# Kernel optimization log

Hardware: AMD Instinct MI355X
Metric: run time of the kernel (lower is better)

## Reference

```python
import jax, jax.numpy as jnp
import numpy as np

D_MODEL = 1024
N_HEAD = 16


def setup_inputs() -> dict:
    key = jax.random.key(0)
    ks = jax.random.split(key, 9)
    d = D_MODEL
    s = 0.02
    return {
        "x": jax.random.normal(ks[0], (4, 2048, d), dtype=jnp.float32),
        "w_q": jax.random.normal(ks[1], (d, d), dtype=jnp.float32) * s,
        "b_q": jax.random.normal(ks[2], (d,), dtype=jnp.float32) * s,
        "w_k": jax.random.normal(ks[3], (d, d), dtype=jnp.float32) * s,
        "b_k": jax.random.normal(ks[4], (d,), dtype=jnp.float32) * s,
        "w_v": jax.random.normal(ks[5], (d, d), dtype=jnp.float32) * s,
        "b_v": jax.random.normal(ks[6], (d,), dtype=jnp.float32) * s,
        "w_o": jax.random.normal(ks[7], (d, d), dtype=jnp.float32) * s,
        "b_o": jax.random.normal(ks[8], (d,), dtype=jnp.float32) * s,
    }


def reference(x, w_q, b_q, w_k, b_k, w_v, b_v, w_o, b_o):
    B, S, D = x.shape
    H = N_HEAD
    dh = D // H

    def split(t):  # [B,S,D] -> [B,H,S,dh]
        return t.reshape(B, S, H, dh).transpose(0, 2, 1, 3)

    q = split(x @ w_q + b_q)
    k = split(x @ w_k + b_k)
    v = split(x @ w_v + b_v)

    scale = 1.0 / jnp.sqrt(jnp.float32(dh))
    score = jnp.einsum("bhqd,bhkd->bhqk", q, k) * scale
    score = jax.nn.softmax(score, axis=-1)
    out = jnp.einsum("bhqk,bhkd->bhqd", score, v)
    out = out.transpose(0, 2, 1, 3).reshape(B, S, D)
    return out @ w_o + b_o
```

## Files before the change

### kernel.cpp

```cpp
#include <hip/hip_runtime.h>


typedef __bf16 bf16x8 __attribute__((ext_vector_type(8)));
typedef __bf16 bf16x4 __attribute__((ext_vector_type(4)));
typedef float f32x4 __attribute__((ext_vector_type(4)));
typedef unsigned short u16x8 __attribute__((ext_vector_type(8)));

#define SEQ 2048
#define DM 1024
#define NHEAD 16
#define MTOT 8192

__device__ __forceinline__ unsigned short f2bf(float f) {
  unsigned u = __builtin_bit_cast(unsigned, f);
  u += 0x7fffu + ((u >> 16) & 1u);
  return (unsigned short)(u >> 16);
}

__device__ __forceinline__ void async16(const void* g, void* l) {
  __builtin_amdgcn_global_load_lds(
      (const __attribute__((address_space(1))) void*)g,
      (__attribute__((address_space(3))) void*)l, 16, 0, 0);
}

__global__ __launch_bounds__(256) void k_cvt(const float* __restrict__ x,
                                             unsigned short* __restrict__ xb) {
  size_t i = ((size_t)blockIdx.x * 256 + threadIdx.x) * 8;
  float4 a = *(const float4*)(x + i);
  float4 b = *(const float4*)(x + i + 4);
  u16x8 o;
  o[0] = f2bf(a.x); o[1] = f2bf(a.y); o[2] = f2bf(a.z); o[3] = f2bf(a.w);
  o[4] = f2bf(b.x); o[5] = f2bf(b.y); o[6] = f2bf(b.z); o[7] = f2bf(b.w);
  *(u16x8*)(xb + i) = o;
}

__global__ __launch_bounds__(256) void k_wt(const float* __restrict__ w0, const float* __restrict__ w1,
                                            const float* __restrict__ w2, const float* __restrict__ w3,
                                            unsigned short* __restrict__ t0, unsigned short* __restrict__ t1,
                                            unsigned short* __restrict__ t2, unsigned short* __restrict__ t3) {
  __shared__ float t[64][65];
  int z = blockIdx.z;
  const float* w = z == 0 ? w0 : z == 1 ? w1 : z == 2 ? w2 : w3;
  unsigned short* wt = z == 0 ? t0 : z == 1 ? t1 : z == 2 ? t2 : t3;
  int nt = blockIdx.x, kt = blockIdx.y;
  int tx = threadIdx.x & 63, ty = threadIdx.x >> 6;
  for (int i = 0; i < 16; ++i) {
    int r = i * 4 + ty;
    t[r][tx] = w[(size_t)(kt * 64 + r) * DM + nt * 64 + tx];
  }
  __syncthreads();
  for (int i = 0; i < 16; ++i) {
    int r = i * 4 + ty;
    wt[(size_t)(nt * 64 + r) * DM + kt * 64 + tx] = f2bf(t[tx][r]);
  }
}

__device__ __forceinline__ void gemm_body(const unsigned short* __restrict__ A,
                                          const unsigned short* __restrict__ Bt,
                                          const float* __restrict__ bias,
                                          unsigned short* __restrict__ Cb,
                                          float* __restrict__ Cf, int bm, int bn) {
  __shared__ __align__(16) unsigned short As[128 * 64];
  __shared__ __align__(16) unsigned short Bs[128 * 64];
  const int K = DM, N = DM;
  int tid = threadIdx.x, w = tid >> 6, l = tid & 63;
  int g = l >> 4, l15 = l & 15;
  int wm = (w >> 1) * 64, wn = (w & 1) * 64;
  f32x4 acc[4][4];
#pragma unroll
  for (int mi = 0; mi < 4; ++mi)
#pragma unroll
    for (int ni = 0; ni < 4; ++ni)
#pragma unroll
      for (int e = 0; e < 4; ++e) acc[mi][ni][e] = 0.f;

  int lr8 = l >> 3, lp = l & 7;
  for (int kt = 0; kt < K / 64; ++kt) {
    __syncthreads();
#pragma unroll
    for (int i = 0; i < 4; ++i) {
      int cs = i * 4 + w;
      int row = cs * 8 + lr8;
      int c = lp ^ lr8;
      async16(A + (size_t)(bm + row) * K + kt * 64 + c * 8, &As[cs * 512]);
      async16(Bt + (size_t)(bn + row) * K + kt * 64 + c * 8, &Bs[cs * 512]);
    }
    __syncthreads();
    bf16x8 af[4][2];
#pragma unroll
    for (int mi = 0; mi < 4; ++mi)
#pragma unroll
      for (int kk = 0; kk < 2; ++kk) {
        int row = wm + mi * 16 + l15;
        af[mi][kk] = *(const bf16x8*)&As[row * 64 + (((kk * 4 + g) ^ (row & 7)) * 8)];
      }
    __builtin_amdgcn_s_setprio(1);
#pragma unroll
    for (int ni = 0; ni < 4; ++ni) {
      int row = wn + ni * 16 + l15;
      bf16x8 b0 = *(const bf16x8*)&Bs[row * 64 + (((0 + g) ^ (row & 7)) * 8)];
      bf16x8 b1 = *(const bf16x8*)&Bs[row * 64 + (((4 + g) ^ (row & 7)) * 8)];
#pragma unroll
      for (int mi = 0; mi < 4; ++mi) {
        acc[mi][ni] = __builtin_amdgcn_mfma_f32_16x16x32_bf16(af[mi][0], b0, acc[mi][ni], 0, 0, 0);
        acc[mi][ni] = __builtin_amdgcn_mfma_f32_16x16x32_bf16(af[mi][1], b1, acc[mi][ni], 0, 0, 0);
      }
    }
    __builtin_amdgcn_s_setprio(0);
  }
  float bv[4];
#pragma unroll
  for (int ni = 0; ni < 4; ++ni) bv[ni] = bias[bn + wn + ni * 16 + l15];
#pragma unroll
  for (int mi = 0; mi < 4; ++mi)
#pragma unroll
    for (int ni = 0; ni < 4; ++ni) {
      int col = bn + wn + ni * 16 + l15;
#pragma unroll
      for (int r = 0; r < 4; ++r) {
        int rowg = bm + wm + mi * 16 + g * 4 + r;
        float v = acc[mi][ni][r] + bv[ni];
        if (Cf) Cf[(size_t)rowg * N + col] = v;
        else    Cb[(size_t)rowg * N + col] = f2bf(v);
      }
    }
}

__global__ __launch_bounds__(256) void k_gemm(const unsigned short* __restrict__ A,
                                              const unsigned short* __restrict__ Bt,
                                              const float* __restrict__ bias,
                                              unsigned short* __restrict__ Cb,
                                              float* __restrict__ Cf) {
  gemm_body(A, Bt, bias, Cb, Cf, blockIdx.y * 128, blockIdx.x * 128);
}

__global__ __launch_bounds__(256) void k_gemm_qkv(const unsigned short* __restrict__ A,
                                                  const unsigned short* bt0, const unsigned short* bt1,
                                                  const unsigned short* bt2,
                                                  const float* b0, const float* b1, const float* b2,
                                                  unsigned short* o0, unsigned short* o1,
                                                  unsigned short* o2) {
  int which = blockIdx.x >> 3;
  const unsigned short* Bt = which == 0 ? bt0 : which == 1 ? bt1 : bt2;
  const float* bias = which == 0 ? b0 : which == 1 ? b1 : b2;
  unsigned short* Cb = which == 0 ? o0 : which == 1 ? o1 : o2;
  gemm_body(A, Bt, bias, Cb, nullptr, blockIdx.y * 128, (blockIdx.x & 7) * 128);
}

__global__ __launch_bounds__(256) void k_vt(const unsigned short* __restrict__ V,
                                            unsigned short* __restrict__ Vt) {
  __shared__ __align__(16) unsigned short t[64 * 64];
  int st = blockIdx.x, bh = blockIdx.y;
  int b = bh >> 4, h = bh & 15;
  int tid = threadIdx.x, w = tid >> 6, l = tid & 63;
  for (int i = 0; i < 2; ++i) {
    int cs = i * 4 + w;
    int row = cs * 8 + (l >> 3);
    int c = l & 7;
    async16(V + ((size_t)(b * SEQ + st * 64 + row) * DM + h * 64 + c * 8), &t[cs * 512]);
  }
  __syncthreads();
  for (int p = 0; p < 2; ++p) {
    int d = p * 32 + (tid >> 3);
    int cs = tid & 7;
    u16x8 o;
    for (int j = 0; j < 8; ++j) o[j] = t[(cs * 8 + j) * 64 + d];
    *(u16x8*)(Vt + ((size_t)bh * 64 + d) * SEQ + st * 64 + cs * 8) = o;
  }
}

__global__ __launch_bounds__(256) void k_attn(const unsigned short* __restrict__ Q,
                                              const unsigned short* __restrict__ Kg,
                                              const unsigned short* __restrict__ Vt,
                                              unsigned short* __restrict__ Og) {
  __shared__ __align__(16) unsigned short Ks[2][64 * 64];
  __shared__ __align__(16) unsigned short Vs[2][64 * 64];
  __shared__ __align__(16) unsigned short Ps[128 * 64];
  const float C = 0.18033688011112042f;
  const float THR = 44.3614195558365f;
  int qt = blockIdx.x, bh = blockIdx.y;
  int b = bh >> 4, h = bh & 15;
  int tid = threadIdx.x, w = tid >> 6, l = tid & 63;
  int g = l >> 4, l15 = l & 15, l7 = l15 & 7;
  int q0 = qt * 128 + w * 32;
  int lr8 = l >> 3, lp = l & 7;

  bf16x8 bq[2][2];
#pragma unroll
  for (int qi = 0; qi < 2; ++qi)
#pragma unroll
    for (int kk = 0; kk < 2; ++kk)
      bq[qi][kk] = *(const bf16x8*)(Q + ((size_t)(b * SEQ + q0 + qi * 16 + l15) * DM) +
                                    h * 64 + kk * 32 + g * 8);

  float mrow[2], lrow[2];
  f32x4 oacc[2][4];
#pragma unroll
  for (int qi = 0; qi < 2; ++qi) {
    mrow[qi] = -__builtin_inff();
    lrow[qi] = 0.f;
#pragma unroll
    for (int no = 0; no < 4; ++no)
#pragma unroll
      for (int e = 0; e < 4; ++e) oacc[qi][no][e] = 0.f;
  }

  auto stage = [&](int kt, int bufi) {
#pragma unroll
    for (int i = 0; i < 2; ++i) {
      int cs = i * 4 + w;
      int row = cs * 8 + lr8;
      int c = lp ^ lr8;
      async16(Kg + ((size_t)(b * SEQ + kt * 64 + row) * DM + h * 64 + c * 8), &Ks[bufi][cs * 512]);
      async16(Vt + ((size_t)(bh * 64 + row) * SEQ + kt * 64 + c * 8), &Vs[bufi][cs * 512]);
    }
  };

  stage(0, 0);
  __syncthreads();

  const int NT = SEQ / 64;
  for (int kt = 0; kt < NT; ++kt) {
    int cur = kt & 1;
    if (kt + 1 < NT) stage(kt + 1, cur ^ 1);

    f32x4 sacc[4][2];
#pragma unroll
    for (int ki = 0; ki < 4; ++ki)
#pragma unroll
      for (int qi = 0; qi < 2; ++qi)
#pragma unroll
        for (int e = 0; e < 4; ++e) sacc[ki][qi][e] = 0.f;
    __builtin_amdgcn_s_setprio(1);
#pragma unroll
    for (int ki = 0; ki < 4; ++ki) {
      int row = ki * 16 + l15;
      bf16x8 a0 = *(const bf16x8*)&Ks[cur][row * 64 + (((0 + g) ^ l7) * 8)];
      bf16x8 a1 = *(const bf16x8*)&Ks[cur][row * 64 + (((4 + g) ^ l7) * 8)];
#pragma unroll
      for (int qi = 0; qi < 2; ++qi) {
        sacc[ki][qi] = __builtin_amdgcn_mfma_f32_16x16x32_bf16(a0, bq[qi][0], sacc[ki][qi], 0, 0, 0);
        sacc[ki][qi] = __builtin_amdgcn_mfma_f32_16x16x32_bf16(a1, bq[qi][1], sacc[ki][qi], 0, 0, 0);
      }
    }
    __builtin_amdgcn_s_setprio(0);

    float mx[2];
#pragma unroll
    for (int qi = 0; qi < 2; ++qi) {
      float m0 = sacc[0][qi][0];
#pragma unroll
      for (int ki = 0; ki < 4; ++ki)
#pragma unroll
        for (int r = 0; r < 4; ++r) m0 = fmaxf(m0, sacc[ki][qi][r]);
      m0 = fmaxf(m0, __shfl_xor(m0, 16));
      m0 = fmaxf(m0, __shfl_xor(m0, 32));
      mx[qi] = m0;
    }
    bool need = (mx[0] > mrow[0] + THR) || (mx[1] > mrow[1] + THR);
    if (__any(need ? 1 : 0)) {
      float co[2];
#pragma unroll
      for (int qi = 0; qi < 2; ++qi) {
        float mn = fmaxf(mrow[qi], mx[qi]);
        co[qi] = __builtin_amdgcn_exp2f((mrow[qi] - mn) * C);
        mrow[qi] = mn;
        lrow[qi] *= co[qi];
      }
#pragma unroll
      for (int qi = 0; qi < 2; ++qi)
#pragma unroll
        for (int r = 0; r < 4; ++r) {
          float bc = __shfl(co[qi], g * 4 + r);
#pragma unroll
          for (int no = 0; no < 4; ++no) oacc[qi][no][r] *= bc;
        }
    }
#pragma unroll
    for (int qi = 0; qi < 2; ++qi) {
      float rs = 0.f;
      int rowg = w * 32 + qi * 16 + l15;
#pragma unroll
      for (int ki = 0; ki < 4; ++ki) {
        float p0 = __builtin_amdgcn_exp2f((sacc[ki][qi][0] - mrow[qi]) * C);
        float p1 = __builtin_amdgcn_exp2f((sacc[ki][qi][1] - mrow[qi]) * C);
        float p2 = __builtin_amdgcn_exp2f((sacc[ki][qi][2] - mrow[qi]) * C);
        float p3 = __builtin_amdgcn_exp2f((sacc[ki][qi][3] - mrow[qi]) * C);
        rs += (p0 + p1) + (p2 + p3);
        bf16x4 pk;
        pk[0] = (__bf16)p0; pk[1] = (__bf16)p1; pk[2] = (__bf16)p2; pk[3] = (__bf16)p3;
        int chunk = ki * 2 + (g >> 1);
        *(bf16x4*)&Ps[rowg * 64 + (((chunk ^ l7) << 3) + ((g & 1) << 2))] = pk;
      }
      rs += __shfl_xor(rs, 16);
      rs += __shfl_xor(rs, 32);
      lrow[qi] += rs;
    }

#pragma unroll
    for (int kk = 0; kk < 2; ++kk) {
      bf16x8 pa[2];
#pragma unroll
      for (int qi = 0; qi < 2; ++qi) {
        int rowg = w * 32 + qi * 16 + l15;
        pa[qi] = *(const bf16x8*)&Ps[rowg * 64 + (((kk * 4 + g) ^ l7) << 3)];
      }
      __builtin_amdgcn_s_setprio(1);
#pragma unroll
      for (int no = 0; no < 4; ++no) {
        int row = no * 16 + l15;
        bf16x8 bv = *(const bf16x8*)&Vs[cur][row * 64 + (((kk * 4 + g) ^ l7) * 8)];
#pragma unroll
        for (int qi = 0; qi < 2; ++qi)
          oacc[qi][no] = __builtin_amdgcn_mfma_f32_16x16x32_bf16(pa[qi], bv, oacc[qi][no], 0, 0, 0);
      }
      __builtin_amdgcn_s_setprio(0);
    }
    __syncthreads();
  }

#pragma unroll
  for (int qi = 0; qi < 2; ++qi)
#pragma unroll
    for (int r = 0; r < 4; ++r) {
      float ls = __shfl(lrow[qi], g * 4 + r);
      float inv = 1.f / ls;
      int srow = q0 + qi * 16 + g * 4 + r;
#pragma unroll
      for (int no = 0; no < 4; ++no)
        Og[(size_t)(b * SEQ + srow) * DM + h * 64 + no * 16 + l15] =
            f2bf(oacc[qi][no][r] * inv);
    }
}

extern "C" void kernel_launch(void* const* d_in, const int* in_sizes, int n_in,
                              void* d_out, int out_size, void* d_ws, size_t ws_size,
                              hipStream_t stream) {
  const float* x  = (const float*)d_in[0];
  const float* wq = (const float*)d_in[1];
  const float* bq = (const float*)d_in[2];
  const float* wk = (const float*)d_in[3];
  const float* bk = (const float*)d_in[4];
  const float* wv = (const float*)d_in[5];
  const float* bv = (const float*)d_in[6];
  const float* wo = (const float*)d_in[7];
  const float* bo = (const float*)d_in[8];

  const size_t SZ_X = (size_t)MTOT * DM * 2;
  const size_t SZ_W = (size_t)DM * DM * 2;
  char* ws = (char*)d_ws;
  size_t off = 0;
  unsigned short* xb  = (unsigned short*)(ws + off); off += SZ_X;
  unsigned short* wqT = (unsigned short*)(ws + off); off += SZ_W;
  unsigned short* wkT = (unsigned short*)(ws + off); off += SZ_W;
  unsigned short* wvT = (unsigned short*)(ws + off); off += SZ_W;
  unsigned short* woT = (unsigned short*)(ws + off); off += SZ_W;
  unsigned short* Qb  = (unsigned short*)(ws + off); off += SZ_X;
  unsigned short* Kb  = (unsigned short*)(ws + off); off += SZ_X;
  unsigned short* Vb  = (unsigned short*)(ws + off); off += SZ_X;
  unsigned short* Vtb = (unsigned short*)(ws + off); off += SZ_X;
  unsigned short* Ab  = (unsigned short*)(ws + off); off += SZ_X;
  if (ws_size < off) return;

  k_cvt<<<dim3(4096), dim3(256), 0, stream>>>(x, xb);
  k_wt<<<dim3(16, 16, 4), dim3(256), 0, stream>>>(wq, wk, wv, wo, wqT, wkT, wvT, woT);
  k_gemm_qkv<<<dim3(24, 64), dim3(256), 0, stream>>>(xb, wqT, wkT, wvT, bq, bk, bv, Qb, Kb, Vb);
  k_vt<<<dim3(32, 64), dim3(256), 0, stream>>>(Vb, Vtb);
  k_attn<<<dim3(16, 64), dim3(256), 0, stream>>>(Qb, Kb, Vtb, Ab);
  k_gemm<<<dim3(8, 64), dim3(256), 0, stream>>>(Ab, woT, bo, nullptr, (float*)d_out);
}
```

Measured before the change: 224.0 us.

## Switch attention to 32x32x16 MFMA with register-resident P via lane shuffles

Rewrites the flash-attention kernel to use 32x32x16 bf16 MFMA tiles. With that tile shape each lane owns a single query row, so the row max and row sum need fewer cross-lane shuffles. The P matrix is no longer round-tripped through shared memory; it is packed to bf16 and rearranged into the B-operand layout with xor-32 shuffles. The key loop is unrolled by two to avoid buffer index arithmetic, and the output is staged through LDS so it can be written with coalesced 16-byte stores. This trades LDS traffic and shuffle overhead for more register pressure and cross-lane shuffles.

```diff
diff --git a/kernel.cpp b/kernel.cpp
--- a/kernel.cpp
+++ b/kernel.cpp
@@ -2,9 +2,10 @@
 
 
 typedef __bf16 bf16x8 __attribute__((ext_vector_type(8)));
-typedef __bf16 bf16x4 __attribute__((ext_vector_type(4)));
 typedef float f32x4 __attribute__((ext_vector_type(4)));
+typedef float f32x16 __attribute__((ext_vector_type(16)));
 typedef unsigned short u16x8 __attribute__((ext_vector_type(8)));
+typedef unsigned u32x4 __attribute__((ext_vector_type(4)));
 
 #define SEQ 2048
 #define DM 1024
@@ -15,6 +16,12 @@
   unsigned u = __builtin_bit_cast(unsigned, f);
   u += 0x7fffu + ((u >> 16) & 1u);
   return (unsigned short)(u >> 16);
+}
+
+__device__ __forceinline__ unsigned pkbf(float lo, float hi) {
+  __bf16 a = (__bf16)lo, b = (__bf16)hi;
+  return ((unsigned)__builtin_bit_cast(unsigned short, b) << 16) |
+         __builtin_bit_cast(unsigned short, a);
 }
 
 __device__ __forceinline__ void async16(const void* g, void* l) {
@@ -173,164 +180,170 @@
                                               const unsigned short* __restrict__ Kg,
                                               const unsigned short* __restrict__ Vt,
                                               unsigned short* __restrict__ Og) {
-  __shared__ __align__(16) unsigned short Ks[2][64 * 64];
-  __shared__ __align__(16) unsigned short Vs[2][64 * 64];
-  __shared__ __align__(16) unsigned short Ps[128 * 64];
+  __shared__ __align__(16) unsigned short smem[16384];
   const float C = 0.18033688011112042f;
   const float THR = 44.3614195558365f;
   int qt = blockIdx.x, bh = blockIdx.y;
   int b = bh >> 4, h = bh & 15;
   int tid = threadIdx.x, w = tid >> 6, l = tid & 63;
-  int g = l >> 4, l15 = l & 15, l7 = l15 & 7;
-  int q0 = qt * 128 + w * 32;
+  int l31 = l & 31, hi = l >> 5, l7 = l & 7;
   int lr8 = l >> 3, lp = l & 7;
-
-  bf16x8 bq[2][2];
-#pragma unroll
-  for (int qi = 0; qi < 2; ++qi)
-#pragma unroll
-    for (int kk = 0; kk < 2; ++kk)
-      bq[qi][kk] = *(const bf16x8*)(Q + ((size_t)(b * SEQ + q0 + qi * 16 + l15) * DM) +
-                                    h * 64 + kk * 32 + g * 8);
-
-  float mrow[2], lrow[2];
-  f32x4 oacc[2][4];
-#pragma unroll
-  for (int qi = 0; qi < 2; ++qi) {
-    mrow[qi] = -__builtin_inff();
-    lrow[qi] = 0.f;
-#pragma unroll
-    for (int no = 0; no < 4; ++no)
-#pragma unroll
-      for (int e = 0; e < 4; ++e) oacc[qi][no][e] = 0.f;
-  }
-
-  auto stage = [&](int kt, int bufi) {
+  int q0w = qt * 128 + w * 32;
+  unsigned short* const ks0 = smem;
+  unsigned short* const ks1 = smem + 4096;
+  unsigned short* const vs0 = smem + 8192;
+  unsigned short* const vs1 = smem + 12288;
+
+  bf16x8 qf[4];
+#pragma unroll
+  for (int c = 0; c < 4; ++c)
+    qf[c] = *(const bf16x8*)(Q + (size_t)(b * SEQ + q0w + l31) * DM + h * 64 + c * 16 + hi * 8);
+
+  float mrow = -__builtin_inff(), lrow = 0.f;
+  f32x16 oacc[2];
+#pragma unroll
+  for (int d = 0; d < 2; ++d)
+#pragma unroll
+    for (int r = 0; r < 16; ++r) oacc[d][r] = 0.f;
+
+  auto stage = [&](int kt, unsigned short* kdst, unsigned short* vdst) {
 #pragma unroll
     for (int i = 0; i < 2; ++i) {
       int cs = i * 4 + w;
       int row = cs * 8 + lr8;
       int c = lp ^ lr8;
-      async16(Kg + ((size_t)(b * SEQ + kt * 64 + row) * DM + h * 64 + c * 8), &Ks[bufi][cs * 512]);
-      async16(Vt + ((size_t)(bh * 64 + row) * SEQ + kt * 64 + c * 8), &Vs[bufi][cs * 512]);
+      async16(Kg + ((size_t)(b * SEQ + kt * 64 + row) * DM + h * 64 + c * 8), kdst + cs * 512);
+      async16(Vt + (((size_t)bh * 64 + row) * SEQ + kt * 64 + c * 8), vdst + cs * 512);
     }
   };
 
-  stage(0, 0);
+  auto tile = [&](int kt, unsigned short* kc, unsigned short* vc,
+                  unsigned short* kn, unsigned short* vn) {
+    const int NT = SEQ / 64;
+    if (kt + 1 < NT) stage(kt + 1, kn, vn);
+
+    f32x16 sacc[2];
+#pragma unroll
+    for (int kh = 0; kh < 2; ++kh)
+#pragma unroll
+      for (int r = 0; r < 16; ++r) sacc[kh][r] = 0.f;
+    __builtin_amdgcn_s_setprio(1);
+#pragma unroll
+    for (int kh = 0; kh < 2; ++kh) {
+      const unsigned short* kbase = kc + (kh * 32 + l31) * 64;
+#pragma unroll
+      for (int c = 0; c < 4; ++c) {
+        bf16x8 a = *(const bf16x8*)(kbase + (((c * 2 + hi) ^ l7) << 3));
+        sacc[kh] = __builtin_amdgcn_mfma_f32_32x32x16_bf16(a, qf[c], sacc[kh], 0, 0, 0);
+      }
+    }
+    __builtin_amdgcn_s_setprio(0);
+
+    float mx = sacc[0][0];
+#pragma unroll
+    for (int kh = 0; kh < 2; ++kh)
+#pragma unroll
+      for (int r = 0; r < 16; ++r) mx = fmaxf(mx, sacc[kh][r]);
+    mx = fmaxf(mx, __shfl_xor(mx, 32));
+    if (__any(mx > mrow + THR)) {
+      float mn = fmaxf(mrow, mx);
+      float co = __builtin_amdgcn_exp2f((mrow - mn) * C);
+      lrow *= co;
+      mrow = mn;
+#pragma unroll
+      for (int d = 0; d < 2; ++d)
+#pragma unroll
+        for (int r = 0; r < 16; ++r) oacc[d][r] *= co;
+    }
+    float mC = mrow * C;
+    float rs = 0.f;
+#pragma unroll
+    for (int kh = 0; kh < 2; ++kh)
+#pragma unroll
+      for (int r = 0; r < 16; ++r) {
+        float p = __builtin_amdgcn_exp2f(__builtin_fmaf(sacc[kh][r], C, -mC));
+        sacc[kh][r] = p;
+        rs += p;
+      }
+    rs += __shfl_xor(rs, 32);
+    lrow += rs;
+
+    unsigned pw[16];
+#pragma unroll
+    for (int kh = 0; kh < 2; ++kh)
+#pragma unroll
+      for (int qd = 0; qd < 4; ++qd) {
+        pw[kh * 8 + qd * 2 + 0] = pkbf(sacc[kh][qd * 4 + 0], sacc[kh][qd * 4 + 1]);
+        pw[kh * 8 + qd * 2 + 1] = pkbf(sacc[kh][qd * 4 + 2], sacc[kh][qd * 4 + 3]);
+      }
+    bf16x8 pf[4];
+#pragma unroll
+    for (int ks = 0; ks < 4; ++ks) {
+      int base = (ks >> 1) * 8 + (ks & 1) * 4;
+      unsigned A0 = pw[base + 0], A1 = pw[base + 1];
+      unsigned B0 = pw[base + 2], B1 = pw[base + 3];
+      unsigned sA0 = (unsigned)__shfl_xor((int)A0, 32);
+      unsigned sA1 = (unsigned)__shfl_xor((int)A1, 32);
+      unsigned sB0 = (unsigned)__shfl_xor((int)B0, 32);
+      unsigned sB1 = (unsigned)__shfl_xor((int)B1, 32);
+      u32x4 fr;
+      fr[0] = hi ? sB0 : A0;
+      fr[1] = hi ? sB1 : A1;
+      fr[2] = hi ? B0 : sA0;
+      fr[3] = hi ? B1 : sA1;
+      pf[ks] = __builtin_bit_cast(bf16x8, fr);
+    }
+
+    __builtin_amdgcn_s_setprio(1);
+#pragma unroll
+    for (int d = 0; d < 2; ++d) {
+      const unsigned short* vbase = vc + (d * 32 + l31) * 64;
+#pragma unroll
+      for (int ks = 0; ks < 4; ++ks) {
+        bf16x8 a = *(const bf16x8*)(vbase + (((ks * 2 + hi) ^ l7) << 3));
+        oacc[d] = __builtin_amdgcn_mfma_f32_32x32x16_bf16(a, pf[ks], oacc[d], 0, 0, 0);
+      }
+    }
+    __builtin_amdgcn_s_setprio(0);
+    __syncthreads();
+  };
+
+  stage(0, ks0, vs0);
   __syncthreads();
-
-  const int NT = SEQ / 64;
-  for (int kt = 0; kt < NT; ++kt) {
-    int cur = kt & 1;
-    if (kt + 1 < NT) stage(kt + 1, cur ^ 1);
-
-    f32x4 sacc[4][2];
-#pragma unroll
-    for (int ki = 0; ki < 4; ++ki)
-#pragma unroll
-      for (int qi = 0; qi < 2; ++qi)
-#pragma unroll
-        for (int e = 0; e < 4; ++e) sacc[ki][qi][e] = 0.f;
-    __builtin_amdgcn_s_setprio(1);
-#pragma unroll
-    for (int ki = 0; ki < 4; ++ki) {
-      int row = ki * 16 + l15;
-      bf16x8 a0 = *(const bf16x8*)&Ks[cur][row * 64 + (((0 + g) ^ l7) * 8)];
-      bf16x8 a1 = *(const bf16x8*)&Ks[cur][row * 64 + (((4 + g) ^ l7) * 8)];
-#pragma unroll
-      for (int qi = 0; qi < 2; ++qi) {
-        sacc[ki][qi] = __builtin_amdgcn_mfma_f32_16x16x32_bf16(a0, bq[qi][0], sacc[ki][qi], 0, 0, 0);
-        sacc[ki][qi] = __builtin_amdgcn_mfma_f32_16x16x32_bf16(a1, bq[qi][1], sacc[ki][qi], 0, 0, 0);
-      }
-    }
-    __builtin_amdgcn_s_setprio(0);
-
-    float mx[2];
-#pragma unroll
-    for (int qi = 0; qi < 2; ++qi) {
-      float m0 = sacc[0][qi][0];
-#pragma unroll
-      for (int ki = 0; ki < 4; ++ki)
-#pragma unroll
-        for (int r = 0; r < 4; ++r) m0 = fmaxf(m0, sacc[ki][qi][r]);
-      m0 = fmaxf(m0, __shfl_xor(m0, 16));
-      m0 = fmaxf(m0, __shfl_xor(m0, 32));
-      mx[qi] = m0;
-    }
-    bool need = (mx[0] > mrow[0] + THR) || (mx[1] > mrow[1] + THR);
-    if (__any(need ? 1 : 0)) {
-      float co[2];
-#pragma unroll
-      for (int qi = 0; qi < 2; ++qi) {
-        float mn = fmaxf(mrow[qi], mx[qi]);
-        co[qi] = __builtin_amdgcn_exp2f((mrow[qi] - mn) * C);
-        mrow[qi] = mn;
-        lrow[qi] *= co[qi];
-      }
-#pragma unroll
-      for (int qi = 0; qi < 2; ++qi)
-#pragma unroll
-        for (int r = 0; r < 4; ++r) {
-          float bc = __shfl(co[qi], g * 4 + r);
-#pragma unroll
-          for (int no = 0; no < 4; ++no) oacc[qi][no][r] *= bc;
-        }
-    }
-#pragma unroll
-    for (int qi = 0; qi < 2; ++qi) {
-      float rs = 0.f;
-      int rowg = w * 32 + qi * 16 + l15;
-#pragma unroll
-      for (int ki = 0; ki < 4; ++ki) {
-        float p0 = __builtin_amdgcn_exp2f((sacc[ki][qi][0] - mrow[qi]) * C);
-        float p1 = __builtin_amdgcn_exp2f((sacc[ki][qi][1] - mrow[qi]) * C);
-        float p2 = __builtin_amdgcn_exp2f((sacc[ki][qi][2] - mrow[qi]) * C);
-        float p3 = __builtin_amdgcn_exp2f((sacc[ki][qi][3] - mrow[qi]) * C);
-        rs += (p0 + p1) + (p2 + p3);
-        bf16x4 pk;
-        pk[0] = (__bf16)p0; pk[1] = (__bf16)p1; pk[2] = (__bf16)p2; pk[3] = (__bf16)p3;
-        int chunk = ki * 2 + (g >> 1);
-        *(bf16x4*)&Ps[rowg * 64 + (((chunk ^ l7) << 3) + ((g & 1) << 2))] = pk;
-      }
-      rs += __shfl_xor(rs, 16);
-      rs += __shfl_xor(rs, 32);
-      lrow[qi] += rs;
-    }
-
-#pragma unroll
-    for (int kk = 0; kk < 2; ++kk) {
-      bf16x8 pa[2];
-#pragma unroll
-      for (int qi = 0; qi < 2; ++qi) {
-        int rowg = w * 32 + qi * 16 + l15;
-        pa[qi] = *(const bf16x8*)&Ps[rowg * 64 + (((kk * 4 + g) ^ l7) << 3)];
-      }
-      __builtin_amdgcn_s_setprio(1);
-#pragma unroll
-      for (int no = 0; no < 4; ++no) {
-        int row = no * 16 + l15;
-        bf16x8 bv = *(const bf16x8*)&Vs[cur][row * 64 + (((kk * 4 + g) ^ l7) * 8)];
-#pragma unroll
-        for (int qi = 0; qi < 2; ++qi)
-          oacc[qi][no] = __builtin_amdgcn_mfma_f32_16x16x32_bf16(pa[qi], bv, oacc[qi][no], 0, 0, 0);
-      }
-      __builtin_amdgcn_s_setprio(0);
-    }
-    __syncthreads();
-  }
-
-#pragma unroll
-  for (int qi = 0; qi < 2; ++qi)
-#pragma unroll
-    for (int r = 0; r < 4; ++r) {
-      float ls = __shfl(lrow[qi], g * 4 + r);
-      float inv = 1.f / ls;
-      int srow = q0 + qi * 16 + g * 4 + r;
-#pragma unroll
-      for (int no = 0; no < 4; ++no)
-        Og[(size_t)(b * SEQ + srow) * DM + h * 64 + no * 16 + l15] =
-            f2bf(oacc[qi][no][r] * inv);
-    }
+  for (int kt = 0; kt < SEQ / 64; kt += 2) {
+    tile(kt, ks0, vs0, ks1, vs1);
+    tile(kt + 1, ks1, vs1, ks0, vs0);
+  }
+
+  float inv = 1.f / lrow;
+  unsigned* ot32 = (unsigned*)(smem + w * (32 * 66));
+#pragma unroll
+  for (int d = 0; d < 2; ++d)
+#pragma unroll
+    for (int qd = 0; qd < 4; ++qd) {
+      unsigned u0 = pkbf(oacc[d][qd * 4 + 0] * inv, oacc[d][qd * 4 + 1] * inv);
+      unsigned u1 = pkbf(oacc[d][qd * 4 + 2] * inv, oacc[d][qd * 4 + 3] * inv);
+      int idx = l31 * 33 + d * 16 + qd * 4 + hi * 2;
+      ot32[idx] = u0;
+      ot32[idx + 1] = u1;
+    }
+  __syncthreads();
+  {
+    int row = l >> 1, half = l & 1;
+    const unsigned* src = ot32 - (w * (32 * 66) / 2) + (w * (32 * 66) / 2);
+    const unsigned* sr = (const unsigned*)(smem + w * (32 * 66)) + row * 33 + half * 16;
+    (void)src;
+    unsigned o[16];
+#pragma unroll
+    for (int j = 0; j < 16; ++j) o[j] = sr[j];
+    size_t gbase = (size_t)(b * SEQ + q0w + row) * DM + h * 64 + half * 32;
+#pragma unroll
+    for (int i = 0; i < 4; ++i) {
+      u32x4 t;
+      t[0] = o[i * 4 + 0]; t[1] = o[i * 4 + 1]; t[2] = o[i * 4 + 2]; t[3] = o[i * 4 + 3];
+      *(u32x4*)(Og + gbase + i * 8) = t;
+    }
+  }
 }
 
 extern "C" void kernel_launch(void* const* d_in, const int* in_sizes, int n_in,
```

New measurement: 214.3 us. 1.05x faster.
